# Kernel tuning notes

Measured on AMD Instinct MI355X. Metric: run time of the kernel, lower is better.

## Reference

```python
import jax, jax.numpy as jnp
import numpy as np

TOTAL_BITS = 16
FRAC_BITS = 8
SCALE = float(2 ** FRAC_BITS)
MINV = -(2.0 ** (TOTAL_BITS - 1)) / SCALE          # -128.0
MAXV = (2.0 ** (TOTAL_BITS - 1) - 1.0) / SCALE     # 127.99609375
BN_EPS = 1e-5


def fp_quantize(x):
    """Fixed-point fake-quant: clamp to representable range, round to nearest
    multiple of 2^-frac_bits. Rounding uses straight-through estimator (matches
    the repo's RoundToFixedPoint autograd)."""
    x = jnp.clip(x, MINV, MAXV)
    r = jnp.round(x * SCALE) / SCALE
    return x + jax.lax.stop_gradient(r - x)


def setup_inputs() -> dict:
    key = jax.random.key(0)
    k1, k2, k3 = jax.random.split(key, 3)
    B, IN, OUT = 8192, 2048, 2048
    x = jax.random.normal(k1, (B, IN), dtype=jnp.float32)
    # realistic init scale so fixed-point range is exercised but not saturated
    weight = jax.random.normal(k2, (OUT, IN), dtype=jnp.float32) * 0.02
    bias = jax.random.normal(k3, (OUT,), dtype=jnp.float32) * 0.02
    gamma = jnp.ones((OUT,), dtype=jnp.float32)
    beta = jnp.zeros((OUT,), dtype=jnp.float32)
    return {"x": x, "weight": weight, "bias": bias, "gamma": gamma, "beta": beta}


def reference(x, weight, bias, gamma, beta):
    # fixed-point Linear: quantize params, quantized matmul, quantized add
    qw = fp_quantize(weight)            # [OUT, IN]
    qb = fp_quantize(bias)              # [OUT]
    y = fp_quantize(x @ qw.T)           # [B, OUT], arithmetics.matmul
    y = fp_quantize(y + qb)             # arithmetics.add
    # BatchNorm1d, training mode: biased batch statistics over the batch dim
    mean = jnp.mean(y, axis=0)
    var = jnp.mean((y - mean) ** 2, axis=0)
    y = (y - mean) * jax.lax.rsqrt(var + BN_EPS)
    y = gamma * y + beta
    # final quantize of BN output
    return fp_quantize(y)
```

## Files before the change

### kernel.cpp

```cpp
#include <hip/hip_runtime.h>
#include <hip/hip_bf16.h>

#define Mdim 8192
#define Ndim 2048
#define Kdim 2048
#define NT   32

constexpr float kMin = -128.0f;
constexpr float kMax = 127.99609375f;
constexpr float kScale = 256.0f;
constexpr float kInvScale = 1.0f / 256.0f;
constexpr float kEps = 1e-5f;

typedef __attribute__((ext_vector_type(8))) short short8;
typedef __attribute__((ext_vector_type(4))) float f32x4;

__device__ __forceinline__ float fpq(float x) {
    x = fminf(fmaxf(x, kMin), kMax);
    return rintf(x * kScale) * kInvScale;
}

__device__ __forceinline__ unsigned short f2bf(float f) {
    union { __hip_bfloat16 h; unsigned short u; } cv;
    cv.h = __float2bfloat16(f);
    return cv.u;
}

__device__ __forceinline__ void gload_lds16(const void* g, void* l) {
    __builtin_amdgcn_global_load_lds(
        (const __attribute__((address_space(1))) unsigned int*)g,
        (__attribute__((address_space(3))) unsigned int*)l,
        16, 0, 0);
}

__device__ __forceinline__ void phase_barrier() {
    __builtin_amdgcn_sched_barrier(0);
    __builtin_amdgcn_s_barrier();
    __builtin_amdgcn_sched_barrier(0);
    asm volatile("" ::: "memory");
}

__device__ __forceinline__ void wait_vmcnt4() {
    __builtin_amdgcn_sched_barrier(0);
    asm volatile("s_waitcnt vmcnt(4)" ::: "memory");
    __builtin_amdgcn_sched_barrier(0);
}

__global__ void fpbn_quant_w(const float* __restrict__ w,
                             unsigned short* __restrict__ wb, int n4) {
    int i = blockIdx.x * blockDim.x + threadIdx.x;
    int stride = gridDim.x * blockDim.x;
    for (; i < n4; i += stride) {
        float4 v = ((const float4*)w)[i];
        ushort4 o;
        o.x = f2bf(fpq(v.x));
        o.y = f2bf(fpq(v.y));
        o.z = f2bf(fpq(v.z));
        o.w = f2bf(fpq(v.w));
        ((ushort4*)wb)[i] = o;
    }
}

__global__ void fpbn_quant_x(const float* __restrict__ x,
                             unsigned short* __restrict__ xb, int n8) {
    int i = blockIdx.x * blockDim.x + threadIdx.x;
    int stride = gridDim.x * blockDim.x;
    for (; i < n8; i += stride) {
        float4 a = ((const float4*)x)[2 * i];
        float4 b = ((const float4*)x)[2 * i + 1];
        uint4 o;
        o.x = (unsigned)f2bf(a.x) | ((unsigned)f2bf(a.y) << 16);
        o.y = (unsigned)f2bf(a.z) | ((unsigned)f2bf(a.w) << 16);
        o.z = (unsigned)f2bf(b.x) | ((unsigned)f2bf(b.y) << 16);
        o.w = (unsigned)f2bf(b.z) | ((unsigned)f2bf(b.w) << 16);
        ((uint4*)xb)[i] = o;
    }
}

template <bool OUT16>
__global__ __launch_bounds__(512, 2) void fpbn_gemm8(
    const unsigned short* __restrict__ xb, const unsigned short* __restrict__ wb,
    const float* __restrict__ bias, short* __restrict__ y16,
    float* __restrict__ yf, float* __restrict__ colsum,
    float* __restrict__ colsumsq) {

    __shared__ unsigned short lds[65536];

    const int t    = threadIdx.x;
    const int lane = t & 63;
    const int w    = t >> 6;
    const int wm   = w >> 2;
    const int wn   = w & 3;

    const int bn   = blockIdx.x & 7;
    const int bm   = blockIdx.x >> 3;
    const int row0 = bm * 256;
    const int col0 = bn * 256;

    const int roff = t >> 3;
    const int colE = ((t & 7) ^ (roff & 7)) * 8;
    const unsigned short* srcA[2] = {
        xb + (size_t)(row0 +   0 + roff) * Kdim + colE,
        xb + (size_t)(row0 + 128 + roff) * Kdim + colE };
    const unsigned short* srcB[2] = {
        wb + (size_t)(col0 +   0 + roff) * Kdim + colE,
        wb + (size_t)(col0 + 128 + roff) * Kdim + colE };
    const int t8 = t * 8;

    const int x3    = lane & 7;
    const int xk    = x3 >> 2;
    const int xh    = x3 & 3;
    const int hi    = lane >> 4;
    const int rb2   = (lane & 15) * 64 + ((hi ^ xh) * 8);
    const int k0off = xk * 32;
    const int k1off = 32 - k0off;
    const int bnoff = (wn & 1) * 4096;

#define STAGE(BUF_, S_, OP_, HALF_) do {                                      \
        int ss_ = (S_) < NT ? (S_) : (S_) - 2;  \
        const unsigned short* sp_ = (OP_ ? srcB : srcA)[HALF_] + ss_ * 64;    \
        unsigned short* dp_ =                                                 \
            &lds[(((BUF_) * 4 + (OP_) * 2 + (HALF_)) << 13) + t8];            \
        gload_lds16(sp_, dp_);                                                \
        gload_lds16(sp_ + (size_t)64 * Kdim, dp_ + 4096);                     \
    } while (0)

#define READA(BUF_, M_, KOFF_) \
    (*(const short8*)&lds[(((BUF_) * 4 + wm) << 13) + rb2 + (M_) * 1024 + (KOFF_)])
#define READB(BUF_, N_, KOFF_) \
    (*(const short8*)&lds[(((BUF_) * 4 + 2 + (wn >> 1)) << 13) + bnoff + rb2 + (N_) * 1024 + (KOFF_)])
#define MFMA_(A_, B_, C_) \
    C_ = __builtin_amdgcn_mfma_f32_16x16x32_bf16(A_, B_, C_, 0, 0, 0)

    f32x4 acc[8][4] = {};

    STAGE(0, 0, 0, 0); STAGE(0, 0, 0, 1); STAGE(0, 0, 1, 0); STAGE(0, 0, 1, 1);
    STAGE(1, 1, 0, 0); STAGE(1, 1, 0, 1);
    wait_vmcnt4();
    phase_barrier();

#define KTILE(BUF_, ST1_, ST2_, ST3_, ST4_) do {                              \
        _Pragma("unroll") for (int m = 0; m < 4; ++m) {                       \
            Af[m][0] = READA(BUF_, m, k0off);                                 \
            Af[m][1] = READA(BUF_, m, k1off); }                               \
        _Pragma("unroll") for (int n = 0; n < 2; ++n) {                       \
            Bf0[n][0] = READB(BUF_, n, k0off);                                \
            Bf0[n][1] = READB(BUF_, n, k1off); }                              \
        ST1_;                                                                 \
        phase_barrier();                                                      \
        __builtin_amdgcn_s_setprio(1);                                        \
        _Pragma("unroll") for (int m = 0; m < 4; ++m)                         \
        _Pragma("unroll") for (int n = 0; n < 2; ++n) {                       \
            MFMA_(Af[m][0], Bf0[n][0], acc[m][n]);                            \
            MFMA_(Af[m][1], Bf0[n][1], acc[m][n]); }                          \
        __builtin_amdgcn_s_setprio(0);                                        \
        phase_barrier();                                                      \
                                                                      \
        _Pragma("unroll") for (int m = 0; m < 4; ++m) {                       \
            Af2[m][0] = READA(BUF_, m + 4, k0off);                            \
            Af2[m][1] = READA(BUF_, m + 4, k1off); }                          \
        _Pragma("unroll") for (int n = 0; n < 2; ++n) {                       \
            Bf1[n][0] = READB(BUF_, n + 2, k0off);                            \
            Bf1[n][1] = READB(BUF_, n + 2, k1off); }                          \
        ST2_;                                                                 \
        phase_barrier();                                                      \
        __builtin_amdgcn_s_setprio(1);                                        \
        _Pragma("unroll") for (int m = 0; m < 4; ++m)                         \
        _Pragma("unroll") for (int n = 0; n < 2; ++n) {                       \
            MFMA_(Af[m][0], Bf1[n][0], acc[m][n + 2]);                        \
            MFMA_(Af[m][1], Bf1[n][1], acc[m][n + 2]); }                      \
        __builtin_amdgcn_s_setprio(0);                                        \
        phase_barrier();                                                      \
                                                                      \
        ST3_;                                                                 \
        phase_barrier();                                                      \
        __builtin_amdgcn_s_setprio(1);                                        \
        _Pragma("unroll") for (int m = 0; m < 4; ++m)                         \
        _Pragma("unroll") for (int n = 0; n < 2; ++n) {                       \
            MFMA_(Af2[m][0], Bf1[n][0], acc[m + 4][n + 2]);                   \
            MFMA_(Af2[m][1], Bf1[n][1], acc[m + 4][n + 2]); }                 \
        __builtin_amdgcn_s_setprio(0);                                        \
        phase_barrier();                                                      \
                                                                      \
        _Pragma("unroll") for (int n = 0; n < 2; ++n) {                       \
            Bf0[n][0] = READB(BUF_, n, k0off);                                \
            Bf0[n][1] = READB(BUF_, n, k1off); }                              \
        ST4_;                                                                 \
        phase_barrier();                                                      \
        __builtin_amdgcn_s_setprio(1);                                        \
        _Pragma("unroll") for (int m = 0; m < 4; ++m)                         \
        _Pragma("unroll") for (int n = 0; n < 2; ++n) {                       \
            MFMA_(Af2[m][0], Bf0[n][0], acc[m + 4][n]);                       \
            MFMA_(Af2[m][1], Bf0[n][1], acc[m + 4][n]); }                     \
        __builtin_amdgcn_s_setprio(0);                                        \
        wait_vmcnt4();                                                        \
        phase_barrier();                                                      \
    } while (0)

#pragma unroll 1
    for (int it = 0; it < NT / 2; ++it) {
        const int s0 = 2 * it;
        short8 Af[4][2], Af2[4][2], Bf0[2][2], Bf1[2][2];
        KTILE(0, STAGE(1, s0 + 1, 1, 0), STAGE(1, s0 + 1, 1, 1),
                 STAGE(0, s0 + 2, 0, 0), STAGE(0, s0 + 2, 0, 1));
        KTILE(1, STAGE(0, s0 + 2, 1, 0), STAGE(0, s0 + 2, 1, 1),
                 STAGE(1, s0 + 3, 0, 0), STAGE(1, s0 + 3, 0, 1));
    }

#pragma unroll
    for (int n = 0; n < 4; ++n) {
        const int col = col0 + wn * 64 + n * 16 + (lane & 15);
        const float qb = fpq(bias[col]);
        float s = 0.0f, s2 = 0.0f;
#pragma unroll
        for (int m = 0; m < 8; ++m) {
            const int rowb = row0 + wm * 128 + m * 16 + ((lane >> 4) * 4);
#pragma unroll
            for (int j = 0; j < 4; ++j) {
                float v = fpq(acc[m][n][j]);
                v = fpq(v + qb);
                if constexpr (OUT16)
                    y16[(size_t)(rowb + j) * Ndim + col] = (short)(v * 256.0f);
                else
                    yf[(size_t)(rowb + j) * Ndim + col] = v;
                s += v;
                s2 += v * v;
            }
        }
        s  += __shfl_xor(s, 16, 64);  s  += __shfl_xor(s, 32, 64);
        s2 += __shfl_xor(s2, 16, 64); s2 += __shfl_xor(s2, 32, 64);
        if (lane < 16) {
            atomicAdd(&colsum[col], s);
            atomicAdd(&colsumsq[col], s2);
        }
    }
#undef STAGE
#undef READA
#undef READB
#undef MFMA_
#undef KTILE
}

__global__ void fpbn_finalize(const float* __restrict__ colsum,
                              const float* __restrict__ colsumsq,
                              const float* __restrict__ gamma,
                              const float* __restrict__ beta,
                              float* __restrict__ a, float* __restrict__ b) {
    int i = blockIdx.x * blockDim.x + threadIdx.x;
    if (i < Ndim) {
        float mean = colsum[i] * (1.0f / Mdim);
        float var  = colsumsq[i] * (1.0f / Mdim) - mean * mean;
        float inv  = 1.0f / sqrtf(var + kEps);
        float ai   = gamma[i] * inv;
        a[i] = ai;
        b[i] = beta[i] - mean * ai;
    }
}

__global__ void fpbn_apply16(const short* __restrict__ y16,
                             float* __restrict__ out,
                             const float* __restrict__ a,
                             const float* __restrict__ b, int n8) {
    int i = blockIdx.x * blockDim.x + threadIdx.x;
    int stride = gridDim.x * blockDim.x;
    for (; i < n8; i += stride) {
        int4 raw = ((const int4*)y16)[i];
        const short* sp = (const short*)&raw;
        int cb = (i * 8) & (Ndim - 1);
        float4 a0 = *(const float4*)&a[cb], a1 = *(const float4*)&a[cb + 4];
        float4 b0 = *(const float4*)&b[cb], b1 = *(const float4*)&b[cb + 4];
        float4 o0, o1;
        o0.x = fpq(fmaf(a0.x, (float)sp[0] * kInvScale, b0.x));
        o0.y = fpq(fmaf(a0.y, (float)sp[1] * kInvScale, b0.y));
        o0.z = fpq(fmaf(a0.z, (float)sp[2] * kInvScale, b0.z));
        o0.w = fpq(fmaf(a0.w, (float)sp[3] * kInvScale, b0.w));
        o1.x = fpq(fmaf(a1.x, (float)sp[4] * kInvScale, b1.x));
        o1.y = fpq(fmaf(a1.y, (float)sp[5] * kInvScale, b1.y));
        o1.z = fpq(fmaf(a1.z, (float)sp[6] * kInvScale, b1.z));
        o1.w = fpq(fmaf(a1.w, (float)sp[7] * kInvScale, b1.w));
        ((float4*)out)[2 * i]     = o0;
        ((float4*)out)[2 * i + 1] = o1;
    }
}

__global__ void fpbn_apply(float* __restrict__ y,
                           const float* __restrict__ a,
                           const float* __restrict__ b, int n4) {
    int i = blockIdx.x * blockDim.x + threadIdx.x;
    int stride = gridDim.x * blockDim.x;
    for (; i < n4; i += stride) {
        float4 v = ((float4*)y)[i];
        int cb = (i * 4) & (Ndim - 1);
        float4 av = *(const float4*)&a[cb];
        float4 bv = *(const float4*)&b[cb];
        v.x = fpq(fmaf(av.x, v.x, bv.x));
        v.y = fpq(fmaf(av.y, v.y, bv.y));
        v.z = fpq(fmaf(av.z, v.z, bv.z));
        v.w = fpq(fmaf(av.w, v.w, bv.w));
        ((float4*)y)[i] = v;
    }
}

extern "C" void kernel_launch(void* const* d_in, const int* in_sizes, int n_in,
                              void* d_out, int out_size, void* d_ws, size_t ws_size,
                              hipStream_t stream) {
    const float* x      = (const float*)d_in[0];
    const float* weight = (const float*)d_in[1];
    const float* bias   = (const float*)d_in[2];
    const float* gamma  = (const float*)d_in[3];
    const float* beta   = (const float*)d_in[4];
    float* out = (float*)d_out;

    char* ws = (char*)d_ws;
    unsigned short* wb = (unsigned short*)ws;
    const size_t wbBytes = (size_t)Ndim * Kdim * 2;
    float* colsum   = (float*)(ws + wbBytes);
    float* colsumsq = colsum + Ndim;
    float* aArr     = colsum + 2 * Ndim;
    float* bArr     = colsum + 3 * Ndim;
    const size_t xbOff = wbBytes + 65536;
    unsigned short* xb = (unsigned short*)(ws + xbOff);
    const size_t xbBytes  = (size_t)Mdim * Kdim * 2;
    const size_t y16Off   = xbOff + xbBytes;
    short* y16 = (short*)(ws + y16Off);
    const size_t need16 = y16Off + (size_t)Mdim * Ndim * 2;

    hipMemsetAsync(colsum, 0, 2 * Ndim * sizeof(float), stream);

    fpbn_quant_w<<<1024, 256, 0, stream>>>(weight, wb, Ndim * Kdim / 4);
    fpbn_quant_x<<<2048, 256, 0, stream>>>(x, xb, Mdim * Kdim / 8);

    if (ws_size >= need16) {
        fpbn_gemm8<true><<<(Mdim / 256) * (Ndim / 256), 512, 0, stream>>>(
            xb, wb, bias, y16, nullptr, colsum, colsumsq);
        fpbn_finalize<<<(Ndim + 255) / 256, 256, 0, stream>>>(
            colsum, colsumsq, gamma, beta, aArr, bArr);
        fpbn_apply16<<<2048, 256, 0, stream>>>(y16, out, aArr, bArr,
                                               Mdim * Ndim / 8);
    } else {
        fpbn_gemm8<false><<<(Mdim / 256) * (Ndim / 256), 512, 0, stream>>>(
            xb, wb, bias, nullptr, out, colsum, colsumsq);
        fpbn_finalize<<<(Ndim + 255) / 256, 256, 0, stream>>>(
            colsum, colsumsq, gamma, beta, aArr, bArr);
        fpbn_apply<<<2048, 256, 0, stream>>>(out, aArr, bArr, Mdim * Ndim / 4);
    }
}
```

Measured before the change: 226.7 us.

## Fuse prep kernels, remap GEMM tiles, trim barriers, and store y16 in fragment order

Merges the memset and the two quantize kernels into one prep launch that also zeroes the column stats. Remaps the GEMM block index so consecutive blocks share weight columns for better L2 reuse. Removes several barriers in the K loop and moves the vmcnt wait, relying on the LDS read order to stay safe. Writes the int16 intermediate in MFMA-fragment order so stores coalesce, and the apply kernel gathers from that layout. The barrier removal and the layout change carry correctness risk and make the apply kernel's reads less contiguous.

```diff
diff --git a/kernel.cpp b/kernel.cpp
--- a/kernel.cpp
+++ b/kernel.cpp
@@ -46,34 +46,40 @@
     __builtin_amdgcn_sched_barrier(0);
 }
 
-__global__ void fpbn_quant_w(const float* __restrict__ w,
-                             unsigned short* __restrict__ wb, int n4) {
-    int i = blockIdx.x * blockDim.x + threadIdx.x;
-    int stride = gridDim.x * blockDim.x;
-    for (; i < n4; i += stride) {
-        float4 v = ((const float4*)w)[i];
-        ushort4 o;
-        o.x = f2bf(fpq(v.x));
-        o.y = f2bf(fpq(v.y));
-        o.z = f2bf(fpq(v.z));
-        o.w = f2bf(fpq(v.w));
-        ((ushort4*)wb)[i] = o;
-    }
-}
-
-__global__ void fpbn_quant_x(const float* __restrict__ x,
-                             unsigned short* __restrict__ xb, int n8) {
-    int i = blockIdx.x * blockDim.x + threadIdx.x;
-    int stride = gridDim.x * blockDim.x;
-    for (; i < n8; i += stride) {
-        float4 a = ((const float4*)x)[2 * i];
-        float4 b = ((const float4*)x)[2 * i + 1];
-        uint4 o;
-        o.x = (unsigned)f2bf(a.x) | ((unsigned)f2bf(a.y) << 16);
-        o.y = (unsigned)f2bf(a.z) | ((unsigned)f2bf(a.w) << 16);
-        o.z = (unsigned)f2bf(b.x) | ((unsigned)f2bf(b.y) << 16);
-        o.w = (unsigned)f2bf(b.z) | ((unsigned)f2bf(b.w) << 16);
-        ((uint4*)xb)[i] = o;
+__global__ void fpbn_prep(const float* __restrict__ w,
+                          unsigned short* __restrict__ wb,
+                          const float* __restrict__ x,
+                          unsigned short* __restrict__ xb,
+                          float* __restrict__ stats) {
+    const int b = blockIdx.x;
+    if (b == 0) {
+        float4 z = {0.f, 0.f, 0.f, 0.f};
+        for (int i = threadIdx.x; i < 1024; i += 256)
+            ((float4*)stats)[i] = z;
+    }
+    if (b < 1024) {
+        const int n4 = Ndim * Kdim / 4;
+        for (int i = b * 256 + threadIdx.x; i < n4; i += 1024 * 256) {
+            float4 v = ((const float4*)w)[i];
+            ushort4 o;
+            o.x = f2bf(fpq(v.x));
+            o.y = f2bf(fpq(v.y));
+            o.z = f2bf(fpq(v.z));
+            o.w = f2bf(fpq(v.w));
+            ((ushort4*)wb)[i] = o;
+        }
+    } else {
+        const int n8 = Mdim * Kdim / 8;
+        for (int i = (b - 1024) * 256 + threadIdx.x; i < n8; i += 2048 * 256) {
+            float4 p = ((const float4*)x)[2 * i];
+            float4 q = ((const float4*)x)[2 * i + 1];
+            uint4 o;
+            o.x = (unsigned)f2bf(p.x) | ((unsigned)f2bf(p.y) << 16);
+            o.y = (unsigned)f2bf(p.z) | ((unsigned)f2bf(p.w) << 16);
+            o.z = (unsigned)f2bf(q.x) | ((unsigned)f2bf(q.y) << 16);
+            o.w = (unsigned)f2bf(q.z) | ((unsigned)f2bf(q.w) << 16);
+            ((uint4*)xb)[i] = o;
+        }
     }
 }
 
@@ -92,8 +98,9 @@
     const int wm   = w >> 2;
     const int wn   = w & 3;
 
-    const int bn   = blockIdx.x & 7;
-    const int bm   = blockIdx.x >> 3;
+    const int blk  = blockIdx.x;
+    const int bm   = (blk & 7) * 4 + (blk >> 6);
+    const int bn   = (blk >> 3) & 7;
     const int row0 = bm * 256;
     const int col0 = bn * 256;
 
@@ -136,18 +143,20 @@
 
     STAGE(0, 0, 0, 0); STAGE(0, 0, 0, 1); STAGE(0, 0, 1, 0); STAGE(0, 0, 1, 1);
     STAGE(1, 1, 0, 0); STAGE(1, 1, 0, 1);
-    wait_vmcnt4();
+    __builtin_amdgcn_sched_barrier(0);
+    asm volatile("s_waitcnt vmcnt(0)" ::: "memory");
+    __builtin_amdgcn_sched_barrier(0);
     phase_barrier();
 
 #define KTILE(BUF_, ST1_, ST2_, ST3_, ST4_) do {                              \
+                                                        \
+        _Pragma("unroll") for (int n = 0; n < 2; ++n) {                       \
+            Bf0[n][0] = READB(BUF_, n, k0off);                                \
+            Bf0[n][1] = READB(BUF_, n, k1off); }                              \
         _Pragma("unroll") for (int m = 0; m < 4; ++m) {                       \
             Af[m][0] = READA(BUF_, m, k0off);                                 \
             Af[m][1] = READA(BUF_, m, k1off); }                               \
-        _Pragma("unroll") for (int n = 0; n < 2; ++n) {                       \
-            Bf0[n][0] = READB(BUF_, n, k0off);                                \
-            Bf0[n][1] = READB(BUF_, n, k1off); }                              \
         ST1_;                                                                 \
-        phase_barrier();                                                      \
         __builtin_amdgcn_s_setprio(1);                                        \
         _Pragma("unroll") for (int m = 0; m < 4; ++m)                         \
         _Pragma("unroll") for (int n = 0; n < 2; ++n) {                       \
@@ -155,15 +164,14 @@
             MFMA_(Af[m][1], Bf0[n][1], acc[m][n]); }                          \
         __builtin_amdgcn_s_setprio(0);                                        \
         phase_barrier();                                                      \
-                                                                      \
+                \
+        _Pragma("unroll") for (int n = 0; n < 2; ++n) {                       \
+            Bf1[n][0] = READB(BUF_, n + 2, k0off);                            \
+            Bf1[n][1] = READB(BUF_, n + 2, k1off); }                          \
         _Pragma("unroll") for (int m = 0; m < 4; ++m) {                       \
             Af2[m][0] = READA(BUF_, m + 4, k0off);                            \
             Af2[m][1] = READA(BUF_, m + 4, k1off); }                          \
-        _Pragma("unroll") for (int n = 0; n < 2; ++n) {                       \
-            Bf1[n][0] = READB(BUF_, n + 2, k0off);                            \
-            Bf1[n][1] = READB(BUF_, n + 2, k1off); }                          \
         ST2_;                                                                 \
-        phase_barrier();                                                      \
         __builtin_amdgcn_s_setprio(1);                                        \
         _Pragma("unroll") for (int m = 0; m < 4; ++m)                         \
         _Pragma("unroll") for (int n = 0; n < 2; ++n) {                       \
@@ -173,7 +181,6 @@
         phase_barrier();                                                      \
                                                                       \
         ST3_;                                                                 \
-        phase_barrier();                                                      \
         __builtin_amdgcn_s_setprio(1);                                        \
         _Pragma("unroll") for (int m = 0; m < 4; ++m)                         \
         _Pragma("unroll") for (int n = 0; n < 2; ++n) {                       \
@@ -181,11 +188,9 @@
             MFMA_(Af2[m][1], Bf1[n][1], acc[m + 4][n + 2]); }                 \
         __builtin_amdgcn_s_setprio(0);                                        \
         phase_barrier();                                                      \
-                                                                      \
-        _Pragma("unroll") for (int n = 0; n < 2; ++n) {                       \
-            Bf0[n][0] = READB(BUF_, n, k0off);                                \
-            Bf0[n][1] = READB(BUF_, n, k1off); }                              \
+                                         \
         ST4_;                                                                 \
+        wait_vmcnt4();                                                        \
         phase_barrier();                                                      \
         __builtin_amdgcn_s_setprio(1);                                        \
         _Pragma("unroll") for (int m = 0; m < 4; ++m)                         \
@@ -193,8 +198,6 @@
             MFMA_(Af2[m][0], Bf0[n][0], acc[m + 4][n]);                       \
             MFMA_(Af2[m][1], Bf0[n][1], acc[m + 4][n]); }                     \
         __builtin_amdgcn_s_setprio(0);                                        \
-        wait_vmcnt4();                                                        \
-        phase_barrier();                                                      \
     } while (0)
 
 #pragma unroll 1
@@ -219,10 +222,13 @@
             for (int j = 0; j < 4; ++j) {
                 float v = fpq(acc[m][n][j]);
                 v = fpq(v + qb);
-                if constexpr (OUT16)
-                    y16[(size_t)(rowb + j) * Ndim + col] = (short)(v * 256.0f);
-                else
+                if constexpr (OUT16) {
+                    size_t idx = ((((size_t)blk * 8 + w) * 4 + n) * 32
+                                  + m * 4 + j) * 64 + lane;
+                    y16[idx] = (short)(v * 256.0f);
+                } else {
                     yf[(size_t)(rowb + j) * Ndim + col] = v;
+                }
                 s += v;
                 s2 += v * v;
             }
@@ -260,15 +266,24 @@
 __global__ void fpbn_apply16(const short* __restrict__ y16,
                              float* __restrict__ out,
                              const float* __restrict__ a,
-                             const float* __restrict__ b, int n8) {
-    int i = blockIdx.x * blockDim.x + threadIdx.x;
+                             const float* __restrict__ b, int ngroups) {
+    int tid = blockIdx.x * blockDim.x + threadIdx.x;
     int stride = gridDim.x * blockDim.x;
-    for (; i < n8; i += stride) {
-        int4 raw = ((const int4*)y16)[i];
+    for (int g = tid; g < ngroups; g += stride) {
+        const int r  = g >> 8;
+        const int c  = (g & 255) * 8;
+        const int bm = r >> 8, wm = (r >> 7) & 1, m = (r >> 4) & 7,
+                  hi = (r >> 2) & 3, j = r & 3;
+        const int bn = c >> 8, wn = (c >> 6) & 3, n = (c >> 4) & 3,
+                  lane = hi * 16 + (c & 15);
+        const int blk = (bm >> 2) | (bn << 3) | ((bm & 3) << 6);
+        const int w   = wm * 4 + wn;
+        const size_t idx = ((((size_t)blk * 8 + w) * 4 + n) * 32
+                            + m * 4 + j) * 64 + lane;
+        int4 raw = *(const int4*)(y16 + idx);
         const short* sp = (const short*)&raw;
-        int cb = (i * 8) & (Ndim - 1);
-        float4 a0 = *(const float4*)&a[cb], a1 = *(const float4*)&a[cb + 4];
-        float4 b0 = *(const float4*)&b[cb], b1 = *(const float4*)&b[cb + 4];
+        float4 a0 = *(const float4*)&a[c], a1 = *(const float4*)&a[c + 4];
+        float4 b0 = *(const float4*)&b[c], b1 = *(const float4*)&b[c + 4];
         float4 o0, o1;
         o0.x = fpq(fmaf(a0.x, (float)sp[0] * kInvScale, b0.x));
         o0.y = fpq(fmaf(a0.y, (float)sp[1] * kInvScale, b0.y));
@@ -278,8 +293,9 @@
         o1.y = fpq(fmaf(a1.y, (float)sp[5] * kInvScale, b1.y));
         o1.z = fpq(fmaf(a1.z, (float)sp[6] * kInvScale, b1.z));
         o1.w = fpq(fmaf(a1.w, (float)sp[7] * kInvScale, b1.w));
-        ((float4*)out)[2 * i]     = o0;
-        ((float4*)out)[2 * i + 1] = o1;
+        float* op = out + (size_t)r * Ndim + c;
+        ((float4*)op)[0] = o0;
+        ((float4*)op)[1] = o1;
     }
 }
 
@@ -325,10 +341,7 @@
     short* y16 = (short*)(ws + y16Off);
     const size_t need16 = y16Off + (size_t)Mdim * Ndim * 2;
 
-    hipMemsetAsync(colsum, 0, 2 * Ndim * sizeof(float), stream);
-
-    fpbn_quant_w<<<1024, 256, 0, stream>>>(weight, wb, Ndim * Kdim / 4);
-    fpbn_quant_x<<<2048, 256, 0, stream>>>(x, xb, Mdim * Kdim / 8);
+    fpbn_prep<<<3072, 256, 0, stream>>>(weight, wb, x, xb, colsum);
 
     if (ws_size >= need16) {
         fpbn_gemm8<true><<<(Mdim / 256) * (Ndim / 256), 512, 0, stream>>>(
```

Result: no change. 230.1 us (+1.5%).
